# Optimization experiments

Measured on AMD Instinct MI355X. Metric: run time of the kernel, lower is better.

The kernel has to match this reference:

```python
import jax, jax.numpy as jnp
import numpy as np

N = 50000      # nodes
E = 800000     # edges (before self-loops)
IN = 128       # in_dim
HID = 64       # hidden_dim
HEADS = 4
OUT = 64       # out_dim
NEG_SLOPE = 0.2
EPS = 1e-16


def gat_conv(x, src, dst, W, att_src, att_dst, b, heads, out_ch, concat):
    """PyG GATConv (eval mode): gather -> attention -> segment softmax -> scatter."""
    n = x.shape[0]
    h = (x @ W).reshape(n, heads, out_ch)                 # [N,H,C]
    a_s = (h * att_src).sum(-1)                           # [N,H]
    a_d = (h * att_dst).sum(-1)                           # [N,H]
    alpha = jax.nn.leaky_relu(a_s[src] + a_d[dst], NEG_SLOPE)   # [E,H]
    amax = jax.ops.segment_max(alpha, dst, num_segments=n)      # stable softmax per dst
    alpha = jnp.exp(alpha - amax[dst])
    denom = jax.ops.segment_sum(alpha, dst, num_segments=n)
    alpha = alpha / (denom[dst] + EPS)
    msg = h[src] * alpha[:, :, None]                      # [E,H,C]
    out = jax.ops.segment_sum(msg, dst, num_segments=n)   # [N,H,C]
    out = out.reshape(n, heads * out_ch) if concat else out.mean(axis=1)
    return out + b


def setup_inputs() -> dict:
    key = jax.random.key(0)
    ks = jax.random.split(key, 16)
    lin = lambda k, fi, fo: jax.random.normal(k, (fi, fo), jnp.float32) / jnp.sqrt(fi)
    x = jax.random.normal(ks[0], (N, IN), jnp.float32)
    edge_index = jax.random.randint(ks[1], (2, E), 0, N, dtype=jnp.int32)
    return {
        "x": x,
        "edge_index": edge_index,
        "W1": lin(ks[2], IN, HEADS * HID),
        "att_src1": jax.random.normal(ks[3], (HEADS, HID)) * 0.1,
        "att_dst1": jax.random.normal(ks[4], (HEADS, HID)) * 0.1,
        "b1": jnp.zeros((HEADS * HID,), jnp.float32),
        "W2": lin(ks[5], HEADS * HID, OUT),
        "att_src2": jax.random.normal(ks[6], (1, OUT)) * 0.1,
        "att_dst2": jax.random.normal(ks[7], (1, OUT)) * 0.1,
        "b2": jnp.zeros((OUT,), jnp.float32),
        "dW1": lin(ks[8], OUT, HID),
        "db1": jnp.zeros((HID,), jnp.float32),
        "dW2": lin(ks[9], HID, IN),
        "db2": jnp.zeros((IN,), jnp.float32),
    }


def reference(x, edge_index, W1, att_src1, att_dst1, b1, W2, att_src2, att_dst2, b2,
              dW1, db1, dW2, db2):
    n = x.shape[0]
    loops = jnp.arange(n, dtype=edge_index.dtype)         # add_self_loops (PyG default)
    src = jnp.concatenate([edge_index[0], loops])
    dst = jnp.concatenate([edge_index[1], loops])
    # encode (dropout is identity in eval mode)
    h = jax.nn.elu(gat_conv(x, src, dst, W1, att_src1, att_dst1, b1, HEADS, HID, True))
    z = gat_conv(h, src, dst, W2, att_src2, att_dst2, b2, 1, OUT, False)
    # F.normalize(z, p=2, dim=-1)
    z = z / jnp.clip(jnp.linalg.norm(z, axis=-1, keepdims=True), 1e-12)
    # feat_decoder: Linear -> ELU -> Linear
    x_hat = jax.nn.elu(z @ dW1 + db1) @ dW2 + db2
    return (z, x_hat)
```

## Files before the change

### kernel.cpp

```cpp
#include <hip/hip_runtime.h>
#include <hip/hip_bf16.h>


#define IN_DIM   128
#define C1       256
#define HEADS    4
#define HID      64
#define OUT_DIM  64

typedef __attribute__((ext_vector_type(8))) short short8;
typedef __attribute__((ext_vector_type(4))) float f32x4;

__device__ __forceinline__ float lrelu(float x) { return x > 0.f ? x : 0.2f * x; }
__device__ __forceinline__ float elu1(float x)  { return x > 0.f ? x : (__expf(x) - 1.f); }
__device__ __forceinline__ float expc(float x)  { return __expf(fminf(x, 60.f)); }
__device__ __forceinline__ float bfu(unsigned int u) {
    union { unsigned int i; float f; } c; c.i = u << 16; return c.f;
}
__device__ __forceinline__ unsigned short pk(float f) {
    union { float f; unsigned int i; } c; c.f = f;
    return (unsigned short)((c.i + 0x7fffu + ((c.i >> 16) & 1u)) >> 16);
}

__global__ __launch_bounds__(256) void w1f_k(const float* __restrict__ W1,
                                             unsigned short* __restrict__ W1f)
{
    const int idx = blockIdx.x * 256 + threadIdx.x;
    if (idx >= 64 * 64) return;
    const int lane = idx & 63, e = idx >> 6;
    const int nt = e >> 2, kc = e & 3, q = lane >> 4, c = lane & 15;
    unsigned short tmp[8];
    #pragma unroll
    for (int j = 0; j < 8; ++j)
        tmp[j] = pk(W1[(kc * 32 + q * 8 + j) * 256 + nt * 16 + c]);
    ushort4* dst = (ushort4*)(W1f + (size_t)idx * 8);
    dst[0] = make_ushort4(tmp[0], tmp[1], tmp[2], tmp[3]);
    dst[1] = make_ushort4(tmp[4], tmp[5], tmp[6], tmp[7]);
}

__global__ __launch_bounds__(256) void w2f_k(const float* __restrict__ W2,
                                             unsigned short* __restrict__ W2f)
{
    const int idx = blockIdx.x * 256 + threadIdx.x;
    if (idx >= 32 * 64) return;
    const int lane = idx & 63, e = idx >> 6;
    const int nt = e >> 3, kc = e & 7, q = lane >> 4, c = lane & 15;
    unsigned short tmp[8];
    #pragma unroll
    for (int j = 0; j < 8; ++j)
        tmp[j] = pk(W2[(kc * 32 + q * 8 + j) * 64 + nt * 16 + c]);
    ushort4* dst = (ushort4*)(W2f + (size_t)idx * 8);
    dst[0] = make_ushort4(tmp[0], tmp[1], tmp[2], tmp[3]);
    dst[1] = make_ushort4(tmp[4], tmp[5], tmp[6], tmp[7]);
}

__global__ __launch_bounds__(256) void gemm1_k(
    const float* __restrict__ x, const unsigned short* __restrict__ W1f,
    const float* __restrict__ as1, const float* __restrict__ ad1,
    unsigned short* __restrict__ h1b, float* __restrict__ a_s1,
    float* __restrict__ a_d1, int N)
{
    __shared__ short lds[64 * 264];
    const int t = threadIdx.x, w = t >> 6, l = t & 63;
    const int q = l >> 4, c = l & 15;
    const int n0 = blockIdx.x * 64;
    for (int i = t; i < 64 * 32; i += 256) {
        const int r = i >> 5, k4 = (i & 31) * 4;
        const int rn = min(n0 + r, N - 1);
        const float4 v = *(const float4*)&x[(size_t)rn * IN_DIM + k4];
        *(ushort4*)&lds[r * 136 + k4] =
            make_ushort4(pk(v.x), pk(v.y), pk(v.z), pk(v.w));
    }
    __syncthreads();
    short8 afr[4];
    const int arow = 16 * w + c;
    #pragma unroll
    for (int kc = 0; kc < 4; ++kc)
        afr[kc] = *(const short8*)&lds[arow * 136 + kc * 32 + q * 8];
    f32x4 acc[16];
    #pragma unroll
    for (int nt = 0; nt < 16; ++nt) acc[nt] = (f32x4){0.f, 0.f, 0.f, 0.f};
    #pragma unroll
    for (int nt = 0; nt < 16; ++nt) {
        #pragma unroll
        for (int kc = 0; kc < 4; ++kc) {
            const short8 bfr =
                *(const short8*)(W1f + ((size_t)(nt * 4 + kc) * 64 + l) * 8);
            acc[nt] = __builtin_amdgcn_mfma_f32_16x16x32_bf16(afr[kc], bfr,
                                                              acc[nt], 0, 0, 0);
        }
    }
    #pragma unroll
    for (int h = 0; h < 4; ++h) {
        float vsr[4] = {0.f, 0.f, 0.f, 0.f}, vdr[4] = {0.f, 0.f, 0.f, 0.f};
        #pragma unroll
        for (int n4 = 0; n4 < 4; ++n4) {
            const int nt = h * 4 + n4;
            const float sa = as1[nt * 16 + c], da = ad1[nt * 16 + c];
            #pragma unroll
            for (int r = 0; r < 4; ++r) {
                vsr[r] += acc[nt][r] * sa;
                vdr[r] += acc[nt][r] * da;
            }
        }
        #pragma unroll
        for (int r = 0; r < 4; ++r) {
            #pragma unroll
            for (int off = 1; off < 16; off <<= 1) {
                vsr[r] += __shfl_xor(vsr[r], off, 64);
                vdr[r] += __shfl_xor(vdr[r], off, 64);
            }
            const int node = n0 + 16 * w + q * 4 + r;
            if (c == 0 && node < N) {
                a_s1[node * 4 + h] = vsr[r];
                a_d1[node * 4 + h] = vdr[r];
            }
        }
    }
    __syncthreads();
    #pragma unroll
    for (int nt = 0; nt < 16; ++nt)
        #pragma unroll
        for (int r = 0; r < 4; ++r)
            lds[(16 * w + q * 4 + r) * 264 + nt * 16 + c] = (short)pk(acc[nt][r]);
    __syncthreads();
    for (int i = t; i < 64 * 32; i += 256) {
        const int r = i >> 5, ch = (i & 31) * 8;
        const int node = n0 + r;
        if (node < N)
            *(short8*)&h1b[(size_t)node * C1 + ch] =
                *(const short8*)&lds[r * 264 + ch];
    }
}

__global__ void deg_k(const int* __restrict__ ei, int E, int Etot,
                      int* __restrict__ rowptr)
{
    const int e = blockIdx.x * blockDim.x + threadIdx.x;
    if (e >= Etot) return;
    const int d = (e < E) ? ei[E + e] : e - E;
    atomicAdd(&rowptr[1 + d], 1);
}

__device__ __forceinline__ int blk_incl_scan(int v, int t) {
    __shared__ int wsum[4];
    const int lane = t & 63, wid = t >> 6;
    int s = v;
    #pragma unroll
    for (int off = 1; off < 64; off <<= 1) {
        const int u = __shfl_up(s, off, 64);
        if (lane >= off) s += u;
    }
    if (lane == 63) wsum[wid] = s;
    __syncthreads();
    int add = 0;
    #pragma unroll
    for (int k = 0; k < 4; ++k) if (k < wid) add += wsum[k];
    __syncthreads();
    return s + add;
}

__global__ __launch_bounds__(256) void scanA_k(const int* __restrict__ rowptr,
                                               int* __restrict__ psum, int N)
{
    const int t = threadIdx.x;
    const int i = blockIdx.x * 256 + t;
    int v = (i < N) ? rowptr[1 + i] : 0;
    #pragma unroll
    for (int off = 1; off < 64; off <<= 1) v += __shfl_xor(v, off, 64);
    __shared__ int ws[4];
    if ((t & 63) == 0) ws[t >> 6] = v;
    __syncthreads();
    if (t == 0) psum[blockIdx.x] = ws[0] + ws[1] + ws[2] + ws[3];
}

__global__ __launch_bounds__(256) void scanB_k(int* __restrict__ psum, int SC)
{
    const int t = threadIdx.x;
    const int v = (t < SC) ? psum[t] : 0;
    const int inc = blk_incl_scan(v, t);
    if (t < SC) psum[t] = inc - v;
}

__global__ __launch_bounds__(256) void scanC_k(int* __restrict__ rowptr,
                                               int* __restrict__ cursor,
                                               const int* __restrict__ psum, int N)
{
    const int t = threadIdx.x;
    const int i = blockIdx.x * 256 + t;
    const int v = (i < N) ? rowptr[1 + i] : 0;
    const int inc = blk_incl_scan(v, t);
    const int base = psum[blockIdx.x];
    if (i < N) {
        rowptr[1 + i] = base + inc;
        cursor[i]     = base + inc - v;
    }
}

__global__ void fill_k(const int* __restrict__ ei, int E, int Etot,
                       int* __restrict__ cursor, int* __restrict__ col,
                       int* __restrict__ row)
{
    const int e = blockIdx.x * blockDim.x + threadIdx.x;
    if (e >= Etot) return;
    int s, d;
    if (e < E) { s = ei[e]; d = ei[E + e]; } else { s = d = e - E; }
    const int pos = atomicAdd(&cursor[d], 1);
    col[pos] = s;
    row[pos] = d;
}

__global__ void ew1_k(const int* __restrict__ col, const int* __restrict__ row,
                      const float* __restrict__ a_s1, const float* __restrict__ a_d1,
                      float* __restrict__ ew1, int Etot)
{
    const int p = blockIdx.x * blockDim.x + threadIdx.x;
    if (p >= Etot) return;
    const int s = col[p], d = row[p];
    const float4 sv = *(const float4*)&a_s1[s * 4];
    const float4 dv = *(const float4*)&a_d1[d * 4];
    float4 w;
    w.x = expc(lrelu(sv.x + dv.x));
    w.y = expc(lrelu(sv.y + dv.y));
    w.z = expc(lrelu(sv.z + dv.z));
    w.w = expc(lrelu(sv.w + dv.w));
    *(float4*)&ew1[(size_t)p * 4] = w;
}

__global__ void ew2_k(const int* __restrict__ col, const int* __restrict__ row,
                      const float* __restrict__ a_s2, const float* __restrict__ a_d2,
                      float* __restrict__ ew2, int Etot)
{
    const int p = blockIdx.x * blockDim.x + threadIdx.x;
    if (p >= Etot) return;
    ew2[p] = expc(lrelu(a_s2[col[p]] + a_d2[row[p]]));
}

__global__ __launch_bounds__(256) void agg1_k(
    const int* __restrict__ rowptr, const int* __restrict__ col,
    const float* __restrict__ ew1, const unsigned short* __restrict__ h1b,
    const float* __restrict__ b1, unsigned short* __restrict__ hxb, int N)
{
    const int t = threadIdx.x, w = t >> 6, l = t & 63;
    const int n = blockIdx.x * 4 + w;
    if (n >= N) return;
    const int beg = rowptr[n], end = rowptr[n + 1];
    const int head = l >> 4;
    float a0 = 0.f, a1 = 0.f, a2 = 0.f, a3 = 0.f, wsum = 0.f;
    for (int t0 = beg; t0 < end; t0 += 16) {
        const int m = min(16, end - t0);
        const int pe = t0 + (l & 15);
        const int   scol = (pe < end) ? col[pe] : 0;
        const float wst  = (pe < end) ? ew1[(size_t)pe * 4 + head] : 0.f;
        for (int j0 = 0; j0 < m; j0 += 8) {
            ushort4 hv[8]; float wu[8];
            #pragma unroll
            for (int u = 0; u < 8; ++u) {
                const int su = __shfl(scol, j0 + u, 64);
                wu[u] = __shfl(wst, (l & 48) + j0 + u, 64);
                hv[u] = *(const ushort4*)(h1b + (size_t)su * C1 + 4 * l);
            }
            #pragma unroll
            for (int u = 0; u < 8; ++u) {
                a0 = fmaf(bfu(hv[u].x), wu[u], a0);
                a1 = fmaf(bfu(hv[u].y), wu[u], a1);
                a2 = fmaf(bfu(hv[u].z), wu[u], a2);
                a3 = fmaf(bfu(hv[u].w), wu[u], a3);
                wsum += wu[u];
            }
        }
    }
    const float4 bb = *(const float4*)&b1[4 * l];
    const float inv = 1.f / (wsum + 1e-16f);
    ushort4 o;
    o.x = pk(elu1(a0 * inv + bb.x));
    o.y = pk(elu1(a1 * inv + bb.y));
    o.z = pk(elu1(a2 * inv + bb.z));
    o.w = pk(elu1(a3 * inv + bb.w));
    *(ushort4*)&hxb[(size_t)n * C1 + 4 * l] = o;
}

__global__ __launch_bounds__(256) void gemm2_k(
    const unsigned short* __restrict__ hxb, const unsigned short* __restrict__ W2f,
    const float* __restrict__ as2, const float* __restrict__ ad2,
    unsigned short* __restrict__ h2b, float* __restrict__ a_s2,
    float* __restrict__ a_d2, int N)
{
    __shared__ short lds[64 * 264];
    const int t = threadIdx.x, w = t >> 6, l = t & 63;
    const int q = l >> 4, c = l & 15;
    const int n0 = blockIdx.x * 64;
    for (int i = t; i < 64 * 32; i += 256) {
        const int r = i >> 5, ch = (i & 31) * 8;
        const int rn = min(n0 + r, N - 1);
        *(short8*)&lds[r * 264 + ch] =
            *(const short8*)&hxb[(size_t)rn * C1 + ch];
    }
    __syncthreads();
    short8 afr[8];
    const int arow = 16 * w + c;
    #pragma unroll
    for (int kc = 0; kc < 8; ++kc)
        afr[kc] = *(const short8*)&lds[arow * 264 + kc * 32 + q * 8];
    f32x4 acc[4];
    #pragma unroll
    for (int nt = 0; nt < 4; ++nt) acc[nt] = (f32x4){0.f, 0.f, 0.f, 0.f};
    #pragma unroll
    for (int nt = 0; nt < 4; ++nt) {
        #pragma unroll
        for (int kc = 0; kc < 8; ++kc) {
            const short8 bfr =
                *(const short8*)(W2f + ((size_t)(nt * 8 + kc) * 64 + l) * 8);
            acc[nt] = __builtin_amdgcn_mfma_f32_16x16x32_bf16(afr[kc], bfr,
                                                              acc[nt], 0, 0, 0);
        }
    }
    {
        float vsr[4] = {0.f, 0.f, 0.f, 0.f}, vdr[4] = {0.f, 0.f, 0.f, 0.f};
        #pragma unroll
        for (int nt = 0; nt < 4; ++nt) {
            const float sa = as2[nt * 16 + c], da = ad2[nt * 16 + c];
            #pragma unroll
            for (int r = 0; r < 4; ++r) {
                vsr[r] += acc[nt][r] * sa;
                vdr[r] += acc[nt][r] * da;
            }
        }
        #pragma unroll
        for (int r = 0; r < 4; ++r) {
            #pragma unroll
            for (int off = 1; off < 16; off <<= 1) {
                vsr[r] += __shfl_xor(vsr[r], off, 64);
                vdr[r] += __shfl_xor(vdr[r], off, 64);
            }
            const int node = n0 + 16 * w + q * 4 + r;
            if (c == 0 && node < N) {
                a_s2[node] = vsr[r];
                a_d2[node] = vdr[r];
            }
        }
    }
    __syncthreads();
    #pragma unroll
    for (int nt = 0; nt < 4; ++nt)
        #pragma unroll
        for (int r = 0; r < 4; ++r)
            lds[(16 * w + q * 4 + r) * 72 + nt * 16 + c] = (short)pk(acc[nt][r]);
    __syncthreads();
    for (int i = t; i < 64 * 8; i += 256) {
        const int r = i >> 3, ch = (i & 7) * 8;
        const int node = n0 + r;
        if (node < N)
            *(short8*)&h2b[(size_t)node * OUT_DIM + ch] =
                *(const short8*)&lds[r * 72 + ch];
    }
}

__global__ __launch_bounds__(256) void agg2_k(
    const int* __restrict__ rowptr, const int* __restrict__ col,
    const float* __restrict__ ew2, const unsigned short* __restrict__ h2b,
    const float* __restrict__ b2, float* __restrict__ zout, int N)
{
    const int t = threadIdx.x, w = t >> 6, l = t & 63;
    const int n = blockIdx.x * 4 + w;
    if (n >= N) return;
    const int beg = rowptr[n], end = rowptr[n + 1];
    const int half = l >> 5, c2 = l & 31;
    float a0 = 0.f, a1 = 0.f, wsum = 0.f;
    for (int t0 = beg; t0 < end; t0 += 64) {
        const int m = min(64, end - t0);
        const int p = t0 + l;
        const int   scol = (p < end) ? col[p] : 0;
        const float wv   = (p < end) ? ew2[p] : 0.f;
        const int pairs = (m + 1) >> 1;
        for (int j0 = 0; j0 < pairs; j0 += 8) {
            unsigned int hv[8]; float wu[8];
            #pragma unroll
            for (int u = 0; u < 8; ++u) {
                const int e = 2 * (j0 + u) + half;
                const int su = __shfl(scol, e, 64);
                wu[u] = __shfl(wv, e, 64);
                hv[u] = *(const unsigned int*)(h2b + (size_t)su * OUT_DIM + 2 * c2);
            }
            #pragma unroll
            for (int u = 0; u < 8; ++u) {
                a0 = fmaf(bfu(hv[u] & 0xffffu), wu[u], a0);
                a1 = fmaf(bfu(hv[u] >> 16), wu[u], a1);
                wsum += wu[u];
            }
        }
    }
    a0   += __shfl_xor(a0, 32, 64);
    a1   += __shfl_xor(a1, 32, 64);
    wsum += __shfl_xor(wsum, 32, 64);
    const float inv = 1.f / (wsum + 1e-16f);
    float z0 = a0 * inv + b2[2 * c2];
    float z1 = a1 * inv + b2[2 * c2 + 1];
    float sq = z0 * z0 + z1 * z1;
    #pragma unroll
    for (int off = 1; off < 32; off <<= 1) sq += __shfl_xor(sq, off, 64);
    const float rn = 1.f / fmaxf(sqrtf(sq), 1e-12f);
    if (l < 32) {
        float2 o; o.x = z0 * rn; o.y = z1 * rn;
        *(float2*)&zout[(size_t)n * OUT_DIM + 2 * c2] = o;
    }
}

__global__ __launch_bounds__(256) void dec_k(
    const float* __restrict__ z,
    const float* __restrict__ dW1, const float* __restrict__ db1,
    const float* __restrict__ dW2, const float* __restrict__ db2,
    float* __restrict__ xhat, int N)
{
    __shared__ float zs[32 * 64];
    __shared__ float ts[32 * 64];
    const int t = threadIdx.x;
    const int n0 = blockIdx.x * 32;
    for (int i = t; i < 32 * 64; i += 256) {
        const int nb_l = i >> 6, k = i & 63;
        const int n = min(n0 + nb_l, N - 1);
        zs[(nb_l >> 3) * 512 + k * 8 + (nb_l & 7)] = z[(size_t)n * OUT_DIM + k];
    }
    __syncthreads();
    const int w = t >> 6, l = t & 63;
    const float* zw = zs + w * 512;
    float* tw = ts + w * 512;
    float acc[8] = {0.f, 0.f, 0.f, 0.f, 0.f, 0.f, 0.f, 0.f};
    #pragma unroll 4
    for (int k = 0; k < 64; ++k) {
        const float wv = dW1[k * HID + l];
        const float4 xa = *(const float4*)&zw[k * 8];
        const float4 xb = *(const float4*)&zw[k * 8 + 4];
        acc[0] += xa.x * wv; acc[1] += xa.y * wv;
        acc[2] += xa.z * wv; acc[3] += xa.w * wv;
        acc[4] += xb.x * wv; acc[5] += xb.y * wv;
        acc[6] += xb.z * wv; acc[7] += xb.w * wv;
    }
    const float bb = db1[l];
    #pragma unroll
    for (int nb = 0; nb < 8; ++nb) tw[l * 8 + nb] = elu1(acc[nb] + bb);
    __syncthreads();
    float a0[8] = {0.f, 0.f, 0.f, 0.f, 0.f, 0.f, 0.f, 0.f};
    float a1[8] = {0.f, 0.f, 0.f, 0.f, 0.f, 0.f, 0.f, 0.f};
    #pragma unroll 2
    for (int k = 0; k < 64; ++k) {
        const float w0 = dW2[k * IN_DIM + l];
        const float w1 = dW2[k * IN_DIM + 64 + l];
        const float4 xa = *(const float4*)&tw[k * 8];
        const float4 xb = *(const float4*)&tw[k * 8 + 4];
        const float xv[8] = {xa.x, xa.y, xa.z, xa.w, xb.x, xb.y, xb.z, xb.w};
        #pragma unroll
        for (int nb = 0; nb < 8; ++nb) {
            a0[nb] += xv[nb] * w0;
            a1[nb] += xv[nb] * w1;
        }
    }
    const float bb0 = db2[l], bb1 = db2[64 + l];
    #pragma unroll
    for (int nb = 0; nb < 8; ++nb) {
        const int n = n0 + w * 8 + nb;
        if (n >= N) break;
        xhat[(size_t)n * IN_DIM + l]      = a0[nb] + bb0;
        xhat[(size_t)n * IN_DIM + 64 + l] = a1[nb] + bb1;
    }
}

extern "C" void kernel_launch(void* const* d_in, const int* in_sizes, int n_in,
                              void* d_out, int out_size, void* d_ws, size_t ws_size,
                              hipStream_t stream)
{
    const float* x   = (const float*)d_in[0];
    const int*   ei  = (const int*)d_in[1];
    const float* W1  = (const float*)d_in[2];
    const float* as1 = (const float*)d_in[3];
    const float* ad1 = (const float*)d_in[4];
    const float* b1  = (const float*)d_in[5];
    const float* W2  = (const float*)d_in[6];
    const float* as2 = (const float*)d_in[7];
    const float* ad2 = (const float*)d_in[8];
    const float* b2  = (const float*)d_in[9];
    const float* dW1 = (const float*)d_in[10];
    const float* db1 = (const float*)d_in[11];
    const float* dW2 = (const float*)d_in[12];
    const float* db2 = (const float*)d_in[13];

    const int N    = in_sizes[0] / IN_DIM;
    const int E    = in_sizes[1] / 2;
    const int Etot = E + N;

    float* ws = (float*)d_ws;
    unsigned short* hxb = (unsigned short*)ws;
    float* a_s1 = ws   + (size_t)N * C1;
    float* a_d1 = a_s1 + (size_t)N * HEADS;
    float* a_s2 = a_d1 + (size_t)N * HEADS;
    float* a_d2 = a_s2 + (size_t)N;
    float* ew1  = a_d2 + (size_t)N;
    float* ew2  = ew1  + (size_t)Etot * HEADS;
    unsigned short* h1b = (unsigned short*)(ew2 + (size_t)Etot);
    unsigned short* h2b = h1b + (size_t)N * C1;
    int* rowptr = (int*)(h2b + (size_t)N * OUT_DIM);
    int* cursor = rowptr + (N + 1);
    int* col    = cursor + N;
    int* row    = col    + Etot;
    int* psum   = row    + Etot;
    unsigned short* W1f = (unsigned short*)(psum + 256);
    unsigned short* W2f = W1f + 64 * 64 * 8;

    const size_t needed = ((size_t)N * 428 + 257 + (size_t)Etot * 7) * 4 + 98304;
    if (ws_size < needed) return;

    hipMemsetAsync(rowptr, 0, (size_t)(N + 1) * sizeof(int), stream);

    const int eblk = (Etot + 255) / 256;
    const int SC   = (N + 255) / 256;
    const int mblk = (N + 63) / 64;
    w1f_k  <<<16, 256, 0, stream>>>(W1, W1f);
    w2f_k  <<<8, 256, 0, stream>>>(W2, W2f);
    gemm1_k<<<mblk, 256, 0, stream>>>(x, W1f, as1, ad1, h1b, a_s1, a_d1, N);
    deg_k  <<<eblk, 256, 0, stream>>>(ei, E, Etot, rowptr);
    scanA_k<<<SC, 256, 0, stream>>>(rowptr, psum, N);
    scanB_k<<<1, 256, 0, stream>>>(psum, SC);
    scanC_k<<<SC, 256, 0, stream>>>(rowptr, cursor, psum, N);
    fill_k <<<eblk, 256, 0, stream>>>(ei, E, Etot, cursor, col, row);
    ew1_k  <<<eblk, 256, 0, stream>>>(col, row, a_s1, a_d1, ew1, Etot);
    agg1_k <<<(N + 3) / 4, 256, 0, stream>>>(rowptr, col, ew1, h1b, b1, hxb, N);
    gemm2_k<<<mblk, 256, 0, stream>>>(hxb, W2f, as2, ad2, h2b, a_s2, a_d2, N);
    ew2_k  <<<eblk, 256, 0, stream>>>(col, row, a_s2, a_d2, ew2, Etot);
    agg2_k <<<(N + 3) / 4, 256, 0, stream>>>(rowptr, col, ew2, h2b, b2,
                                             (float*)d_out, N);
    dec_k  <<<(N + 31) / 32, 256, 0, stream>>>((const float*)d_out, dW1, db1,
                                               dW2, db2,
                                               (float*)d_out + (size_t)N * OUT_DIM, N);
}
```

Before: 381.1 us.

## Fuse preprocessing kernels, single-pass chained scan, and inline edge weights

Merges the weight-fragment conversion and degree counting into one launch. It replaces the three-kernel scan with a decoupled-lookback chained scan that runs inside the gemm1 launch. The fill and ew1 kernels are fused, and the row array is dropped. The layer-2 edge weight is now computed inside agg2 instead of materialised, and agg1 batches 64 columns with a 16-deep gather unroll. These cut launch count and intermediate memory traffic. The chained scan relies on earlier blocks being scheduled first and spins on a status array.

```diff
diff --git a/kernel.cpp b/kernel.cpp
--- a/kernel.cpp
+++ b/kernel.cpp
@@ -22,48 +22,100 @@
     return (unsigned short)((c.i + 0x7fffu + ((c.i >> 16) & 1u)) >> 16);
 }
 
-__global__ __launch_bounds__(256) void w1f_k(const float* __restrict__ W1,
-                                             unsigned short* __restrict__ W1f)
-{
-    const int idx = blockIdx.x * 256 + threadIdx.x;
-    if (idx >= 64 * 64) return;
-    const int lane = idx & 63, e = idx >> 6;
-    const int nt = e >> 2, kc = e & 3, q = lane >> 4, c = lane & 15;
-    unsigned short tmp[8];
-    #pragma unroll
-    for (int j = 0; j < 8; ++j)
-        tmp[j] = pk(W1[(kc * 32 + q * 8 + j) * 256 + nt * 16 + c]);
-    ushort4* dst = (ushort4*)(W1f + (size_t)idx * 8);
-    dst[0] = make_ushort4(tmp[0], tmp[1], tmp[2], tmp[3]);
-    dst[1] = make_ushort4(tmp[4], tmp[5], tmp[6], tmp[7]);
-}
-
-__global__ __launch_bounds__(256) void w2f_k(const float* __restrict__ W2,
-                                             unsigned short* __restrict__ W2f)
-{
-    const int idx = blockIdx.x * 256 + threadIdx.x;
-    if (idx >= 32 * 64) return;
-    const int lane = idx & 63, e = idx >> 6;
-    const int nt = e >> 3, kc = e & 7, q = lane >> 4, c = lane & 15;
-    unsigned short tmp[8];
-    #pragma unroll
-    for (int j = 0; j < 8; ++j)
-        tmp[j] = pk(W2[(kc * 32 + q * 8 + j) * 64 + nt * 16 + c]);
-    ushort4* dst = (ushort4*)(W2f + (size_t)idx * 8);
-    dst[0] = make_ushort4(tmp[0], tmp[1], tmp[2], tmp[3]);
-    dst[1] = make_ushort4(tmp[4], tmp[5], tmp[6], tmp[7]);
-}
-
-__global__ __launch_bounds__(256) void gemm1_k(
+__global__ __launch_bounds__(256) void stage1_k(
+    const float* __restrict__ W1, const float* __restrict__ W2,
+    const int* __restrict__ ei, int E, int Etot,
+    unsigned short* __restrict__ W1f, unsigned short* __restrict__ W2f,
+    int* __restrict__ rowptr)
+{
+    const int b = blockIdx.x, t = threadIdx.x;
+    if (b < 16) {
+        const int idx = b * 256 + t;
+        const int lane = idx & 63, e = idx >> 6;
+        const int nt = e >> 2, kc = e & 3, q = lane >> 4, c = lane & 15;
+        unsigned short tmp[8];
+        #pragma unroll
+        for (int j = 0; j < 8; ++j)
+            tmp[j] = pk(W1[(kc * 32 + q * 8 + j) * 256 + nt * 16 + c]);
+        ushort4* dst = (ushort4*)(W1f + (size_t)idx * 8);
+        dst[0] = make_ushort4(tmp[0], tmp[1], tmp[2], tmp[3]);
+        dst[1] = make_ushort4(tmp[4], tmp[5], tmp[6], tmp[7]);
+    } else if (b < 24) {
+        const int idx = (b - 16) * 256 + t;
+        const int lane = idx & 63, e = idx >> 6;
+        const int nt = e >> 3, kc = e & 7, q = lane >> 4, c = lane & 15;
+        unsigned short tmp[8];
+        #pragma unroll
+        for (int j = 0; j < 8; ++j)
+            tmp[j] = pk(W2[(kc * 32 + q * 8 + j) * 64 + nt * 16 + c]);
+        ushort4* dst = (ushort4*)(W2f + (size_t)idx * 8);
+        dst[0] = make_ushort4(tmp[0], tmp[1], tmp[2], tmp[3]);
+        dst[1] = make_ushort4(tmp[4], tmp[5], tmp[6], tmp[7]);
+    } else {
+        const int e = (b - 24) * 256 + t;
+        if (e < Etot) {
+            const int d = (e < E) ? ei[E + e] : e - E;
+            atomicAdd(&rowptr[1 + d], 1);
+        }
+    }
+}
+
+__device__ __forceinline__ int blk_incl_scan(int v, int t) {
+    __shared__ int wsum[4];
+    const int lane = t & 63, wid = t >> 6;
+    int s = v;
+    #pragma unroll
+    for (int off = 1; off < 64; off <<= 1) {
+        const int u = __shfl_up(s, off, 64);
+        if (lane >= off) s += u;
+    }
+    if (lane == 63) wsum[wid] = s;
+    __syncthreads();
+    int add = 0;
+    #pragma unroll
+    for (int k = 0; k < 4; ++k) if (k < wid) add += wsum[k];
+    __syncthreads();
+    return s + add;
+}
+
+__global__ __launch_bounds__(256) void stage2_k(
+    int* __restrict__ rowptr, int* __restrict__ cursor, int* __restrict__ status,
     const float* __restrict__ x, const unsigned short* __restrict__ W1f,
     const float* __restrict__ as1, const float* __restrict__ ad1,
     unsigned short* __restrict__ h1b, float* __restrict__ a_s1,
-    float* __restrict__ a_d1, int N)
-{
+    float* __restrict__ a_d1, int N, int SC)
+{
+    const int t = threadIdx.x;
+    if ((int)blockIdx.x < SC) {
+        const int chunk = blockIdx.x;
+        const int i = chunk * 256 + t;
+        const int v = (i < N) ? rowptr[1 + i] : 0;
+        const int inc = blk_incl_scan(v, t);
+        __shared__ int sbase;
+        if (t == 255) {
+            int base = 0;
+            if (chunk > 0) {
+                volatile int* st = (volatile int*)status;
+                int s;
+                while ((s = st[chunk - 1]) == 0) { }
+                base = s - 1;
+            }
+            ((volatile int*)status)[chunk] = base + inc + 1;
+            sbase = base;
+        }
+        __syncthreads();
+        const int base = sbase;
+        if (i < N) {
+            rowptr[1 + i] = base + inc;
+            cursor[i]     = base + inc - v;
+        }
+        return;
+    }
     __shared__ short lds[64 * 264];
-    const int t = threadIdx.x, w = t >> 6, l = t & 63;
+    const int bb = blockIdx.x - SC;
+    const int w = t >> 6, l = t & 63;
     const int q = l >> 4, c = l & 15;
-    const int n0 = blockIdx.x * 64;
+    const int n0 = bb * 64;
     for (int i = t; i < 64 * 32; i += 256) {
         const int r = i >> 5, k4 = (i & 31) * 4;
         const int rn = min(n0 + r, N - 1);
@@ -133,73 +185,11 @@
     }
 }
 
-__global__ void deg_k(const int* __restrict__ ei, int E, int Etot,
-                      int* __restrict__ rowptr)
-{
-    const int e = blockIdx.x * blockDim.x + threadIdx.x;
-    if (e >= Etot) return;
-    const int d = (e < E) ? ei[E + e] : e - E;
-    atomicAdd(&rowptr[1 + d], 1);
-}
-
-__device__ __forceinline__ int blk_incl_scan(int v, int t) {
-    __shared__ int wsum[4];
-    const int lane = t & 63, wid = t >> 6;
-    int s = v;
-    #pragma unroll
-    for (int off = 1; off < 64; off <<= 1) {
-        const int u = __shfl_up(s, off, 64);
-        if (lane >= off) s += u;
-    }
-    if (lane == 63) wsum[wid] = s;
-    __syncthreads();
-    int add = 0;
-    #pragma unroll
-    for (int k = 0; k < 4; ++k) if (k < wid) add += wsum[k];
-    __syncthreads();
-    return s + add;
-}
-
-__global__ __launch_bounds__(256) void scanA_k(const int* __restrict__ rowptr,
-                                               int* __restrict__ psum, int N)
-{
-    const int t = threadIdx.x;
-    const int i = blockIdx.x * 256 + t;
-    int v = (i < N) ? rowptr[1 + i] : 0;
-    #pragma unroll
-    for (int off = 1; off < 64; off <<= 1) v += __shfl_xor(v, off, 64);
-    __shared__ int ws[4];
-    if ((t & 63) == 0) ws[t >> 6] = v;
-    __syncthreads();
-    if (t == 0) psum[blockIdx.x] = ws[0] + ws[1] + ws[2] + ws[3];
-}
-
-__global__ __launch_bounds__(256) void scanB_k(int* __restrict__ psum, int SC)
-{
-    const int t = threadIdx.x;
-    const int v = (t < SC) ? psum[t] : 0;
-    const int inc = blk_incl_scan(v, t);
-    if (t < SC) psum[t] = inc - v;
-}
-
-__global__ __launch_bounds__(256) void scanC_k(int* __restrict__ rowptr,
-                                               int* __restrict__ cursor,
-                                               const int* __restrict__ psum, int N)
-{
-    const int t = threadIdx.x;
-    const int i = blockIdx.x * 256 + t;
-    const int v = (i < N) ? rowptr[1 + i] : 0;
-    const int inc = blk_incl_scan(v, t);
-    const int base = psum[blockIdx.x];
-    if (i < N) {
-        rowptr[1 + i] = base + inc;
-        cursor[i]     = base + inc - v;
-    }
-}
-
-__global__ void fill_k(const int* __restrict__ ei, int E, int Etot,
-                       int* __restrict__ cursor, int* __restrict__ col,
-                       int* __restrict__ row)
+__global__ void fill_ew1_k(const int* __restrict__ ei, int E, int Etot,
+                           int* __restrict__ cursor, int* __restrict__ col,
+                           const float* __restrict__ a_s1,
+                           const float* __restrict__ a_d1,
+                           float* __restrict__ ew1)
 {
     const int e = blockIdx.x * blockDim.x + threadIdx.x;
     if (e >= Etot) return;
@@ -207,16 +197,6 @@
     if (e < E) { s = ei[e]; d = ei[E + e]; } else { s = d = e - E; }
     const int pos = atomicAdd(&cursor[d], 1);
     col[pos] = s;
-    row[pos] = d;
-}
-
-__global__ void ew1_k(const int* __restrict__ col, const int* __restrict__ row,
-                      const float* __restrict__ a_s1, const float* __restrict__ a_d1,
-                      float* __restrict__ ew1, int Etot)
-{
-    const int p = blockIdx.x * blockDim.x + threadIdx.x;
-    if (p >= Etot) return;
-    const int s = col[p], d = row[p];
     const float4 sv = *(const float4*)&a_s1[s * 4];
     const float4 dv = *(const float4*)&a_d1[d * 4];
     float4 w;
@@ -224,16 +204,7 @@
     w.y = expc(lrelu(sv.y + dv.y));
     w.z = expc(lrelu(sv.z + dv.z));
     w.w = expc(lrelu(sv.w + dv.w));
-    *(float4*)&ew1[(size_t)p * 4] = w;
-}
-
-__global__ void ew2_k(const int* __restrict__ col, const int* __restrict__ row,
-                      const float* __restrict__ a_s2, const float* __restrict__ a_d2,
-                      float* __restrict__ ew2, int Etot)
-{
-    const int p = blockIdx.x * blockDim.x + threadIdx.x;
-    if (p >= Etot) return;
-    ew2[p] = expc(lrelu(a_s2[col[p]] + a_d2[row[p]]));
+    *(float4*)&ew1[(size_t)pos * 4] = w;
 }
 
 __global__ __launch_bounds__(256) void agg1_k(
@@ -247,21 +218,28 @@
     const int beg = rowptr[n], end = rowptr[n + 1];
     const int head = l >> 4;
     float a0 = 0.f, a1 = 0.f, a2 = 0.f, a3 = 0.f, wsum = 0.f;
-    for (int t0 = beg; t0 < end; t0 += 16) {
-        const int m = min(16, end - t0);
-        const int pe = t0 + (l & 15);
-        const int   scol = (pe < end) ? col[pe] : 0;
-        const float wst  = (pe < end) ? ew1[(size_t)pe * 4 + head] : 0.f;
-        for (int j0 = 0; j0 < m; j0 += 8) {
-            ushort4 hv[8]; float wu[8];
-            #pragma unroll
-            for (int u = 0; u < 8; ++u) {
-                const int su = __shfl(scol, j0 + u, 64);
-                wu[u] = __shfl(wst, (l & 48) + j0 + u, 64);
-                hv[u] = *(const ushort4*)(h1b + (size_t)su * C1 + 4 * l);
-            }
-            #pragma unroll
-            for (int u = 0; u < 8; ++u) {
+    for (int t0 = beg; t0 < end; t0 += 64) {
+        const int m = min(64, end - t0);
+        const int p = t0 + l;
+        const int scol = (p < end) ? col[p] : 0;
+        for (int g = 0; g < m; g += 16) {
+            const int pe = t0 + g + (l & 15);
+            const float wst = (pe < end) ? ew1[(size_t)pe * 4 + head] : 0.f;
+            const int mm = min(16, m - g);
+            ushort4 hv[16]; float wu[16];
+            #pragma unroll
+            for (int u = 0; u < 16; ++u) {
+                if (u < mm) {
+                    const int su = __shfl(scol, g + u, 64);
+                    wu[u] = __shfl(wst, (l & 48) + u, 64);
+                    hv[u] = *(const ushort4*)(h1b + (size_t)su * C1 + 4 * l);
+                } else {
+                    wu[u] = 0.f;
+                    hv[u] = make_ushort4(0, 0, 0, 0);
+                }
+            }
+            #pragma unroll
+            for (int u = 0; u < 16; ++u) {
                 a0 = fmaf(bfu(hv[u].x), wu[u], a0);
                 a1 = fmaf(bfu(hv[u].y), wu[u], a1);
                 a2 = fmaf(bfu(hv[u].z), wu[u], a2);
@@ -358,20 +336,23 @@
 
 __global__ __launch_bounds__(256) void agg2_k(
     const int* __restrict__ rowptr, const int* __restrict__ col,
-    const float* __restrict__ ew2, const unsigned short* __restrict__ h2b,
-    const float* __restrict__ b2, float* __restrict__ zout, int N)
+    const float* __restrict__ a_s2, const float* __restrict__ a_d2,
+    const unsigned short* __restrict__ h2b, const float* __restrict__ b2,
+    float* __restrict__ zout, int N)
 {
     const int t = threadIdx.x, w = t >> 6, l = t & 63;
     const int n = blockIdx.x * 4 + w;
     if (n >= N) return;
     const int beg = rowptr[n], end = rowptr[n + 1];
     const int half = l >> 5, c2 = l & 31;
+    const float ad2n = a_d2[n];
     float a0 = 0.f, a1 = 0.f, wsum = 0.f;
     for (int t0 = beg; t0 < end; t0 += 64) {
         const int m = min(64, end - t0);
         const int p = t0 + l;
-        const int   scol = (p < end) ? col[p] : 0;
-        const float wv   = (p < end) ? ew2[p] : 0.f;
+        const int scol = (p < end) ? col[p] : 0;
+        float wv = 0.f;
+        if (p < end) wv = expc(lrelu(a_s2[scol] + ad2n));
         const int pairs = (m + 1) >> 1;
         for (int j0 = 0; j0 < pairs; j0 += 8) {
             unsigned int hv[8]; float wu[8];
@@ -487,46 +468,45 @@
     const int N    = in_sizes[0] / IN_DIM;
     const int E    = in_sizes[1] / 2;
     const int Etot = E + N;
-
-    float* ws = (float*)d_ws;
-    unsigned short* hxb = (unsigned short*)ws;
-    float* a_s1 = ws   + (size_t)N * C1;
-    float* a_d1 = a_s1 + (size_t)N * HEADS;
-    float* a_s2 = a_d1 + (size_t)N * HEADS;
-    float* a_d2 = a_s2 + (size_t)N;
-    float* ew1  = a_d2 + (size_t)N;
-    float* ew2  = ew1  + (size_t)Etot * HEADS;
-    unsigned short* h1b = (unsigned short*)(ew2 + (size_t)Etot);
-    unsigned short* h2b = h1b + (size_t)N * C1;
-    int* rowptr = (int*)(h2b + (size_t)N * OUT_DIM);
-    int* cursor = rowptr + (N + 1);
-    int* col    = cursor + N;
-    int* row    = col    + Etot;
-    int* psum   = row    + Etot;
-    unsigned short* W1f = (unsigned short*)(psum + 256);
-    unsigned short* W2f = W1f + 64 * 64 * 8;
-
-    const size_t needed = ((size_t)N * 428 + 257 + (size_t)Etot * 7) * 4 + 98304;
-    if (ws_size < needed) return;
-
-    hipMemsetAsync(rowptr, 0, (size_t)(N + 1) * sizeof(int), stream);
+    const int SC   = (N + 255) / 256;
+
+    char* base = (char*)d_ws;
+    size_t off = 0;
+    auto take = [&](size_t bytes) -> char* {
+        off = (off + 63) & ~(size_t)63;
+        char* p = base + off;
+        off += bytes;
+        return p;
+    };
+    unsigned short* hxb = (unsigned short*)take((size_t)N * C1 * 2);
+    float* a_s1 = (float*)take((size_t)N * HEADS * 4);
+    float* a_d1 = (float*)take((size_t)N * HEADS * 4);
+    float* a_s2 = (float*)take((size_t)N * 4);
+    float* a_d2 = (float*)take((size_t)N * 4);
+    float* ew1  = (float*)take((size_t)Etot * HEADS * 4);
+    unsigned short* h1b = (unsigned short*)take((size_t)N * C1 * 2);
+    unsigned short* h2b = (unsigned short*)take((size_t)N * OUT_DIM * 2);
+    int* rowptr = (int*)take((size_t)(N + 1) * 4);
+    int* status = (int*)take((size_t)SC * 4);
+    int* cursor = (int*)take((size_t)N * 4);
+    int* col    = (int*)take((size_t)Etot * 4);
+    unsigned short* W1f = (unsigned short*)take(64 * 64 * 8 * 2);
+    unsigned short* W2f = (unsigned short*)take(32 * 64 * 8 * 2);
+    if (off > ws_size) return;
+
+    const size_t zspan = (size_t)((char*)(status + SC) - (char*)rowptr);
+    hipMemsetAsync(rowptr, 0, zspan, stream);
 
     const int eblk = (Etot + 255) / 256;
-    const int SC   = (N + 255) / 256;
     const int mblk = (N + 63) / 64;
-    w1f_k  <<<16, 256, 0, stream>>>(W1, W1f);
-    w2f_k  <<<8, 256, 0, stream>>>(W2, W2f);
-    gemm1_k<<<mblk, 256, 0, stream>>>(x, W1f, as1, ad1, h1b, a_s1, a_d1, N);
-    deg_k  <<<eblk, 256, 0, stream>>>(ei, E, Etot, rowptr);
-    scanA_k<<<SC, 256, 0, stream>>>(rowptr, psum, N);
-    scanB_k<<<1, 256, 0, stream>>>(psum, SC);
-    scanC_k<<<SC, 256, 0, stream>>>(rowptr, cursor, psum, N);
-    fill_k <<<eblk, 256, 0, stream>>>(ei, E, Etot, cursor, col, row);
-    ew1_k  <<<eblk, 256, 0, stream>>>(col, row, a_s1, a_d1, ew1, Etot);
+    stage1_k<<<24 + eblk, 256, 0, stream>>>(W1, W2, ei, E, Etot, W1f, W2f, rowptr);
+    stage2_k<<<SC + mblk, 256, 0, stream>>>(rowptr, cursor, status,
+                                            x, W1f, as1, ad1, h1b, a_s1, a_d1,
+                                            N, SC);
+    fill_ew1_k<<<eblk, 256, 0, stream>>>(ei, E, Etot, cursor, col, a_s1, a_d1, ew1);
     agg1_k <<<(N + 3) / 4, 256, 0, stream>>>(rowptr, col, ew1, h1b, b1, hxb, N);
     gemm2_k<<<mblk, 256, 0, stream>>>(hxb, W2f, as2, ad2, h2b, a_s2, a_d2, N);
-    ew2_k  <<<eblk, 256, 0, stream>>>(col, row, a_s2, a_d2, ew2, Etot);
-    agg2_k <<<(N + 3) / 4, 256, 0, stream>>>(rowptr, col, ew2, h2b, b2,
+    agg2_k <<<(N + 3) / 4, 256, 0, stream>>>(rowptr, col, a_s2, a_d2, h2b, b2,
                                              (float*)d_out, N);
     dec_k  <<<(N + 31) / 32, 256, 0, stream>>>((const float*)d_out, dW1, db1,
                                                dW2, db2,
```

Measured after the change: 437.0 us. +14.7%, slower.
